# Optimization experiments

Measured on AMD Instinct MI355X. Metric: run time of the kernel, lower is better.

## Reference

```python
import jax, jax.numpy as jnp
import numpy as np

N, E, F_IN, C, H, B = 50000, 1600000, 64, 64, 2, 64
EPS_BN = 1e-5
NEG_SLOPE = 0.2


def setup_inputs() -> dict:
    key = jax.random.key(0)
    ks = jax.random.split(key, 20)
    s_in = 1.0 / np.sqrt(F_IN)
    s_c = 1.0 / np.sqrt(C)
    inp = {
        "x": jax.random.normal(ks[0], (N, F_IN), jnp.float32),
        "edge_index": jax.random.randint(ks[1], (2, E), 0, N, jnp.int32),
        "batch_index": jnp.sort(jax.random.randint(ks[2], (N,), 0, B, jnp.int32)),
        # GAT layer 1
        "W1": jax.random.normal(ks[3], (F_IN, H * C), jnp.float32) * s_in,
        "att_src1": jax.random.normal(ks[4], (H, C), jnp.float32) * s_c,
        "att_dst1": jax.random.normal(ks[5], (H, C), jnp.float32) * s_c,
        "bias1": jnp.zeros((C,), jnp.float32),
        # skip linear
        "skipW": jax.random.normal(ks[6], (F_IN, C), jnp.float32) * s_in,
        "skipb": jnp.zeros((C,), jnp.float32),
        # BN1
        "gamma1": jnp.ones((C,), jnp.float32),
        "beta1": jnp.zeros((C,), jnp.float32),
        # GAT layer 2
        "W2": jax.random.normal(ks[7], (C, H * C), jnp.float32) * s_c,
        "att_src2": jax.random.normal(ks[8], (H, C), jnp.float32) * s_c,
        "att_dst2": jax.random.normal(ks[9], (H, C), jnp.float32) * s_c,
        "bias2": jnp.zeros((C,), jnp.float32),
        # BN2
        "gamma2": jnp.ones((C,), jnp.float32),
        "beta2": jnp.zeros((C,), jnp.float32),
    }
    return inp


def _gat_conv(x, W, att_src, att_dst, bias, src, dst):
    # PyG GATConv with concat=False (mean over heads), self-loops already in src/dst
    n = x.shape[0]
    h = (x @ W).reshape(n, H, C)                           # [N,H,C]
    a_s = jnp.einsum("nhc,hc->nh", h, att_src)              # [N,H]
    a_d = jnp.einsum("nhc,hc->nh", h, att_dst)
    logits = jax.nn.leaky_relu(a_s[src] + a_d[dst], NEG_SLOPE)  # [E,H]
    m = jax.ops.segment_max(logits, dst, num_segments=n)    # scatter-softmax
    e = jnp.exp(logits - m[dst])
    denom = jax.ops.segment_sum(e, dst, num_segments=n)
    alpha = e / denom[dst]                                  # [E,H]
    msg = h[src] * alpha[:, :, None]                        # [E,H,C]
    out = jax.ops.segment_sum(msg, dst, num_segments=n)     # [N,H,C]
    return out.mean(axis=1) + bias                          # concat=False -> head mean


def _bn(x, gamma, beta):
    # BatchNorm1d, training mode (batch statistics, biased var)
    mu = x.mean(axis=0)
    var = x.var(axis=0)
    return (x - mu) * jax.lax.rsqrt(var + EPS_BN) * gamma + beta


def reference(x, edge_index, batch_index, W1, att_src1, att_dst1, bias1,
              skipW, skipb, gamma1, beta1, W2, att_src2, att_dst2, bias2,
              gamma2, beta2):
    n = x.shape[0]
    loops = jnp.arange(n, dtype=edge_index.dtype)
    src = jnp.concatenate([edge_index[0], loops])  # add_self_loops=True (PyG default)
    dst = jnp.concatenate([edge_index[1], loops])

    h = _gat_conv(x, W1, att_src1, att_dst1, bias1, src, dst)
    h = _bn(h, gamma1, beta1)
    h = jax.nn.gelu(h + x @ skipW + skipb)          # dropout = identity (eval)

    h2 = _gat_conv(h, W2, att_src2, att_dst2, bias2, src, dst)
    h2 = _bn(h2, gamma2, beta2)
    h2 = jax.nn.gelu(h2 + h)

    # global_mean_pool
    sums = jax.ops.segment_sum(h2, batch_index, num_segments=B)
    cnts = jax.ops.segment_sum(jnp.ones((n,), h2.dtype), batch_index, num_segments=B)
    return sums / jnp.maximum(cnts, 1.0)[:, None]   # [B, C]
```

## Files before the change

### kernel.cpp

```cpp
#include <hip/hip_runtime.h>
#include <math.h>


__device__ __forceinline__ float lrelu(float x){ return x > 0.f ? x : 0.2f*x; }
__device__ __forceinline__ float gelu_tanh(float x){
  const float k0 = 0.7978845608028654f;
  const float k1 = 0.044715f;
  float t = tanhf(k0 * fmaf(k1*x*x, x, x));
  return 0.5f*x*(1.f + t);
}
__device__ __forceinline__ unsigned short f2bf(float f){
  unsigned int u = __float_as_uint(f);
  u = (u + 0x7fffu + ((u >> 16) & 1u)) >> 16;
  return (unsigned short)u;
}
__device__ __forceinline__ float bf2f(unsigned short u){
  return __uint_as_float((unsigned int)u << 16);
}
__device__ __forceinline__ float bflo(unsigned int u){ return __uint_as_float(u << 16); }
__device__ __forceinline__ float bfhi(unsigned int u){ return __uint_as_float(u & 0xffff0000u); }
__device__ __forceinline__ unsigned int packbf(float a, float b){
  return ((unsigned int)f2bf(b) << 16) | (unsigned int)f2bf(a);
}
__device__ __forceinline__ unsigned char f2fp8(float v){
  return (unsigned char)(__builtin_amdgcn_cvt_pk_fp8_f32(v, v, 0, false) & 0xff);
}
typedef __attribute__((ext_vector_type(2))) float f32x2;

typedef __attribute__((ext_vector_type(8))) short bf16x8;
typedef __attribute__((ext_vector_type(4))) float f32x4;

__global__ void k_zero(float* __restrict__ p, int n){
  int i = blockIdx.x*blockDim.x + threadIdx.x;
  if (i < n) p[i] = 0.f;
}

__global__ void p_hist(const int* __restrict__ dst, int* __restrict__ bhist,
                       int E, int NB){
  __shared__ int lh[512];
  for (int i = threadIdx.x; i < NB; i += blockDim.x) lh[i] = 0;
  __syncthreads();
  int stride = gridDim.x * blockDim.x;
  for (int i = blockIdx.x*blockDim.x + threadIdx.x; i < E; i += stride)
    atomicAdd(&lh[dst[i] >> 7], 1);
  __syncthreads();
  for (int i = threadIdx.x; i < NB; i += blockDim.x)
    if (lh[i]) atomicAdd(&bhist[i], lh[i]);
}

__global__ void p_scan(const int* __restrict__ bhist, int* __restrict__ boff,
                       int* __restrict__ bcur, int* __restrict__ ptr,
                       int NB, int N, int E){
  __shared__ int ls[512];
  int t = threadIdx.x;
  int v = (t < NB) ? bhist[t] : 0;
  ls[t] = v; __syncthreads();
  for (int o = 1; o < 512; o <<= 1){
    int y = (t >= o) ? ls[t-o] : 0;
    __syncthreads();
    ls[t] += y;
    __syncthreads();
  }
  int ex = ls[t] - v;
  if (t < NB){ boff[t] = ex; bcur[t] = ex; }
  if (t == 0){ boff[NB] = E; ptr[N] = E; }
}

#define BIN_CHUNK 2048
__global__ void p_bin(const int* __restrict__ src, const int* __restrict__ dst,
                      int* __restrict__ bcur, unsigned int* __restrict__ recs,
                      int E, int NB){
  __shared__ int lh[512];
  __shared__ int lbase[512];
  int c0 = blockIdx.x * BIN_CHUNK;
  int cnt = min(BIN_CHUNK, E - c0);
  if (cnt <= 0) return;
  int t = threadIdx.x;
  for (int i = t; i < NB; i += blockDim.x) lh[i] = 0;
  __syncthreads();
  for (int i = t; i < cnt; i += blockDim.x)
    atomicAdd(&lh[dst[c0+i] >> 7], 1);
  __syncthreads();
  for (int i = t; i < NB; i += blockDim.x){
    int c = lh[i];
    lbase[i] = (c > 0) ? atomicAdd(&bcur[i], c) : 0;
    lh[i] = 0;
  }
  __syncthreads();
  for (int i = t; i < cnt; i += blockDim.x){
    int d = dst[c0+i];
    int b = d >> 7;
    int p = atomicAdd(&lh[b], 1);
    recs[lbase[b] + p] = ((unsigned int)src[c0+i] << 7) | (unsigned int)(d & 127);
  }
}

__global__ void p_csr(const unsigned int* __restrict__ recs, const int* __restrict__ boff,
                      int* __restrict__ ptr, int* __restrict__ srcs, int N){
  int b = blockIdx.x;
  int r0 = boff[b], r1 = boff[b+1];
  __shared__ int lh[128];
  int t = threadIdx.x;
  if (t < 128) lh[t] = 0;
  __syncthreads();
  for (int i = r0 + t; i < r1; i += 256)
    atomicAdd(&lh[recs[i] & 127u], 1);
  __syncthreads();
  int mycnt = (t < 128) ? lh[t] : 0;
  for (int o = 1; o < 128; o <<= 1){
    int y = (t < 128 && t >= o) ? lh[t-o] : 0;
    __syncthreads();
    if (t < 128) lh[t] += y;
    __syncthreads();
  }
  if (t < 128){
    int excl = lh[t] - mycnt;
    int node = b*128 + t;
    if (node < N) ptr[node] = r0 + excl;
    lh[t] = excl;
  }
  __syncthreads();
  for (int i = r0 + t; i < r1; i += 256){
    unsigned int rec = recs[i];
    int j = rec & 127u;
    int p = atomicAdd(&lh[j], 1);
    srcs[r0 + p] = (int)(rec >> 7);
  }
}

__global__ void k_gemm3(const float* __restrict__ X, const float* __restrict__ Wm,
                        const float* __restrict__ Wsk, const float* __restrict__ att_s,
                        const float* __restrict__ att_d, unsigned char* __restrict__ Hout,
                        unsigned short* __restrict__ skv, float* __restrict__ a_s,
                        float* __restrict__ a_d, int N){
  constexpr int NT = 12;
  __shared__ unsigned short Bl[NT*2*64*8];
  int t = threadIdx.x;
  const int TOT = 64 * 192;
  for (int e = t; e < TOT; e += 256){
    int k = e / 192, c = e % 192;
    float w = (c < 128) ? Wm[(size_t)k*128 + c] : Wsk[(size_t)k*64 + (c-128)];
    int ct = c >> 4;
    int h = k >> 5, kk = k & 31;
    int e2 = ((kk >> 4) << 2) | (kk & 3);
    int l  = (c & 15) | (((kk >> 2) & 3) << 4);
    Bl[(((ct*2 + h)*64) + l)*8 + e2] = f2bf(w);
  }
  __syncthreads();

  int lane = t & 63, wav = t >> 6;
  int m = lane & 15, g = lane >> 4;
  float asv[8], adv[8];
  #pragma unroll
  for (int ct = 0; ct < 8; ct++){ asv[ct] = att_s[ct*16 + m]; adv[ct] = att_d[ct*16 + m]; }

  #pragma unroll
  for (int it = 0; it < 2; it++){
    int rbase = blockIdx.x*128 + it*64 + wav*16;
    if (rbase >= N) break;
    int r = min(rbase + m, N-1);
    const float* xr = X + (size_t)r*64;
    float4 u0 = *(const float4*)(xr + g*4);
    float4 u1 = *(const float4*)(xr + 16 + g*4);
    float4 u2 = *(const float4*)(xr + 32 + g*4);
    float4 u3 = *(const float4*)(xr + 48 + g*4);
    bf16x8 a0, a1;
    a0[0]=(short)f2bf(u0.x); a0[1]=(short)f2bf(u0.y); a0[2]=(short)f2bf(u0.z); a0[3]=(short)f2bf(u0.w);
    a0[4]=(short)f2bf(u1.x); a0[5]=(short)f2bf(u1.y); a0[6]=(short)f2bf(u1.z); a0[7]=(short)f2bf(u1.w);
    a1[0]=(short)f2bf(u2.x); a1[1]=(short)f2bf(u2.y); a1[2]=(short)f2bf(u2.z); a1[3]=(short)f2bf(u2.w);
    a1[4]=(short)f2bf(u3.x); a1[5]=(short)f2bf(u3.y); a1[6]=(short)f2bf(u3.z); a1[7]=(short)f2bf(u3.w);

    f32x4 acc[NT];
    #pragma unroll
    for (int ct = 0; ct < NT; ct++) acc[ct] = (f32x4){0.f,0.f,0.f,0.f};
    #pragma unroll
    for (int ct = 0; ct < NT; ct++){
      bf16x8 b0 = *(const bf16x8*)&Bl[((ct*2+0)*64 + lane)*8];
      bf16x8 b1 = *(const bf16x8*)&Bl[((ct*2+1)*64 + lane)*8];
      acc[ct] = __builtin_amdgcn_mfma_f32_16x16x32_bf16(a0, b0, acc[ct], 0, 0, 0);
      acc[ct] = __builtin_amdgcn_mfma_f32_16x16x32_bf16(a1, b1, acc[ct], 0, 0, 0);
    }

    float ds0[4]={0,0,0,0}, dd0[4]={0,0,0,0}, ds1[4]={0,0,0,0}, dd1[4]={0,0,0,0};
    #pragma unroll
    for (int ct = 0; ct < 8; ct++){
      #pragma unroll
      for (int q = 0; q < 4; q++){
        float v = acc[ct][q];
        if (ct < 4){ ds0[q] = fmaf(v, asv[ct], ds0[q]); dd0[q] = fmaf(v, adv[ct], dd0[q]); }
        else       { ds1[q] = fmaf(v, asv[ct], ds1[q]); dd1[q] = fmaf(v, adv[ct], dd1[q]); }
      }
    }
    #pragma unroll
    for (int off = 1; off < 16; off <<= 1){
      #pragma unroll
      for (int q = 0; q < 4; q++){
        ds0[q] += __shfl_xor(ds0[q], off); dd0[q] += __shfl_xor(dd0[q], off);
        ds1[q] += __shfl_xor(ds1[q], off); dd1[q] += __shfl_xor(dd1[q], off);
      }
    }
    if (m == 0){
      #pragma unroll
      for (int q = 0; q < 4; q++){
        int rr = rbase + g*4 + q;
        if (rr < N){
          float2 s2; s2.x = ds0[q]; s2.y = ds1[q]; ((float2*)a_s)[rr] = s2;
          float2 d2; d2.x = dd0[q]; d2.y = dd1[q]; ((float2*)a_d)[rr] = d2;
        }
      }
    }
    #pragma unroll
    for (int ct = 0; ct < 8; ct++){
      #pragma unroll
      for (int q = 0; q < 4; q++){
        int rr = rbase + g*4 + q;
        if (rr < N) Hout[(size_t)rr*128 + ct*16 + m] = f2fp8(acc[ct][q]);
      }
    }
    #pragma unroll
    for (int ct = 8; ct < NT; ct++){
      #pragma unroll
      for (int q = 0; q < 4; q++){
        int rr = rbase + g*4 + q;
        if (rr < N) skv[(size_t)rr*64 + (ct-8)*16 + m] = f2bf(acc[ct][q]);
      }
    }
  }
}

__global__ void k_gemm2f(const unsigned short* __restrict__ gout, const unsigned short* __restrict__ skv,
                         const float* __restrict__ part, const float* __restrict__ gamma,
                         const float* __restrict__ beta, const float* __restrict__ skb,
                         const float* __restrict__ W2, const float* __restrict__ att_s,
                         const float* __restrict__ att_d,
                         unsigned char* __restrict__ Hout, unsigned short* __restrict__ hmid,
                         float* __restrict__ a_s, float* __restrict__ a_d,
                         int N, float invN){
  constexpr int NT = 8;
  __shared__ unsigned short Bl[NT*2*64*8];
  __shared__ float scs[64], shs[64];
  int t = threadIdx.x;
  if (t < 64){
    float mu  = part[t] * invN;
    float var = fmaxf(part[64+t] * invN - mu*mu, 0.f);
    float sc  = gamma[t] * rsqrtf(var + 1e-5f);
    scs[t] = sc;
    shs[t] = beta[t] - mu*sc + skb[t];
  }
  const int TOT = 64 * 128;
  for (int e = t; e < TOT; e += 256){
    int k = e >> 7, c = e & 127;
    float w = W2[(size_t)k*128 + c];
    int ct = c >> 4;
    int h = k >> 5, kk = k & 31;
    int e2 = ((kk >> 4) << 2) | (kk & 3);
    int l  = (c & 15) | (((kk >> 2) & 3) << 4);
    Bl[(((ct*2 + h)*64) + l)*8 + e2] = f2bf(w);
  }
  __syncthreads();

  int lane = t & 63, wav = t >> 6;
  int m = lane & 15, g = lane >> 4;
  float asv[8], adv[8];
  #pragma unroll
  for (int ct = 0; ct < 8; ct++){ asv[ct] = att_s[ct*16 + m]; adv[ct] = att_d[ct*16 + m]; }

  #pragma unroll
  for (int it = 0; it < 2; it++){
    int rbase = blockIdx.x*128 + it*64 + wav*16;
    if (rbase >= N) break;
    int rm = rbase + m;
    int r = min(rm, N-1);
    const unsigned short* gr = gout + (size_t)r*64;
    const unsigned short* sr = skv + (size_t)r*64;
    float hv[16];
    #pragma unroll
    for (int j = 0; j < 4; j++){
      int c0 = j*16 + g*4;
      uint2 gp = *(const uint2*)(gr + c0);
      uint2 sp = *(const uint2*)(sr + c0);
      float4 sc4 = *(const float4*)(&scs[c0]);
      float4 sh4 = *(const float4*)(&shs[c0]);
      float v0 = gelu_tanh(fmaf(bflo(gp.x), sc4.x, sh4.x) + bflo(sp.x));
      float v1 = gelu_tanh(fmaf(bfhi(gp.x), sc4.y, sh4.y) + bfhi(sp.x));
      float v2 = gelu_tanh(fmaf(bflo(gp.y), sc4.z, sh4.z) + bflo(sp.y));
      float v3 = gelu_tanh(fmaf(bfhi(gp.y), sc4.w, sh4.w) + bfhi(sp.y));
      hv[4*j+0] = v0; hv[4*j+1] = v1; hv[4*j+2] = v2; hv[4*j+3] = v3;
      if (rm < N){
        uint2 hp; hp.x = packbf(v0, v1); hp.y = packbf(v2, v3);
        *(uint2*)(hmid + (size_t)rm*64 + c0) = hp;
      }
    }
    bf16x8 a0, a1;
    #pragma unroll
    for (int i2 = 0; i2 < 8; i2++) a0[i2] = (short)f2bf(hv[i2]);
    #pragma unroll
    for (int i2 = 0; i2 < 8; i2++) a1[i2] = (short)f2bf(hv[8+i2]);

    f32x4 acc[NT];
    #pragma unroll
    for (int ct = 0; ct < NT; ct++) acc[ct] = (f32x4){0.f,0.f,0.f,0.f};
    #pragma unroll
    for (int ct = 0; ct < NT; ct++){
      bf16x8 b0 = *(const bf16x8*)&Bl[((ct*2+0)*64 + lane)*8];
      bf16x8 b1 = *(const bf16x8*)&Bl[((ct*2+1)*64 + lane)*8];
      acc[ct] = __builtin_amdgcn_mfma_f32_16x16x32_bf16(a0, b0, acc[ct], 0, 0, 0);
      acc[ct] = __builtin_amdgcn_mfma_f32_16x16x32_bf16(a1, b1, acc[ct], 0, 0, 0);
    }

    float ds0[4]={0,0,0,0}, dd0[4]={0,0,0,0}, ds1[4]={0,0,0,0}, dd1[4]={0,0,0,0};
    #pragma unroll
    for (int ct = 0; ct < 8; ct++){
      #pragma unroll
      for (int q = 0; q < 4; q++){
        float v = acc[ct][q];
        if (ct < 4){ ds0[q] = fmaf(v, asv[ct], ds0[q]); dd0[q] = fmaf(v, adv[ct], dd0[q]); }
        else       { ds1[q] = fmaf(v, asv[ct], ds1[q]); dd1[q] = fmaf(v, adv[ct], dd1[q]); }
      }
    }
    #pragma unroll
    for (int off = 1; off < 16; off <<= 1){
      #pragma unroll
      for (int q = 0; q < 4; q++){
        ds0[q] += __shfl_xor(ds0[q], off); dd0[q] += __shfl_xor(dd0[q], off);
        ds1[q] += __shfl_xor(ds1[q], off); dd1[q] += __shfl_xor(dd1[q], off);
      }
    }
    if (m == 0){
      #pragma unroll
      for (int q = 0; q < 4; q++){
        int rr = rbase + g*4 + q;
        if (rr < N){
          float2 s2; s2.x = ds0[q]; s2.y = ds1[q]; ((float2*)a_s)[rr] = s2;
          float2 d2; d2.x = dd0[q]; d2.y = dd1[q]; ((float2*)a_d)[rr] = d2;
        }
      }
    }
    #pragma unroll
    for (int ct = 0; ct < 8; ct++){
      #pragma unroll
      for (int q = 0; q < 4; q++){
        int rr = rbase + g*4 + q;
        if (rr < N) Hout[(size_t)rr*128 + ct*16 + m] = f2fp8(acc[ct][q]);
      }
    }
  }
}

__global__ void k_agg(const unsigned char* __restrict__ Hp, const float* __restrict__ a_s,
                      const float* __restrict__ a_d, const int* __restrict__ ptr,
                      const int* __restrict__ srcs, const float* __restrict__ bias,
                      unsigned int* __restrict__ out, int N){
  __shared__ unsigned int sbuf[4][64];
  __shared__ float wbuf[4][2][64];
  int tid = threadIdx.x;
  int wv = tid >> 6;
  int wid = (blockIdx.x*blockDim.x + tid) >> 6;
  int lane = tid & 63;
  if (wid >= N) return;
  int n = wid;
  const char* HB = (const char*)Hp;
  const float2* AS2 = (const float2*)a_s;
  float2 adv = ((const float2*)a_d)[n];
  float2 asv = AS2[n];
  int e0 = ptr[n], e1 = ptr[n+1];
  float w0 = __expf(lrelu(asv.x + adv.x));
  float w1 = __expf(lrelu(asv.y + adv.y));
  unsigned lane2 = (unsigned)lane << 1;
  unsigned int hw = *(const unsigned short*)(HB + (((unsigned)n << 7) | lane2));
  f32x2 hv = __builtin_amdgcn_cvt_pk_f32_fp8((int)hw, false);
  float wsel = (lane < 32) ? w0 : w1;
  float acc0 = hv.x * wsel;
  float acc1 = hv.y * wsel;
  float d0 = 0.f, d1 = 0.f;
  int hsel = lane >> 5;
  for (int base = e0; base < e1; base += 64){
    int i = base + lane;
    float e_0 = 0.f, e_1 = 0.f; unsigned sv = 0;
    if (i < e1){
      sv = (unsigned)srcs[i];
      float2 av = AS2[sv];
      e_0 = __expf(lrelu(av.x + adv.x));
      e_1 = __expf(lrelu(av.y + adv.y));
    }
    d0 += e_0; d1 += e_1;
    sbuf[wv][lane] = sv << 7;
    wbuf[wv][0][lane] = e_0;
    wbuf[wv][1][lane] = e_1;
    int cnt = min(64, e1 - base);
    #pragma unroll 8
    for (int j = 0; j < cnt; j++){
      unsigned off = sbuf[wv][j];
      float wss = wbuf[wv][hsel][j];
      unsigned int hj = *(const unsigned short*)(HB + (off | lane2));
      f32x2 h2 = __builtin_amdgcn_cvt_pk_f32_fp8((int)hj, false);
      acc0 = fmaf(h2.x, wss, acc0);
      acc1 = fmaf(h2.y, wss, acc1);
    }
  }
  #pragma unroll
  for (int o=32;o>0;o>>=1){ d0 += __shfl_xor(d0,o); d1 += __shfl_xor(d1,o); }
  d0 += w0; d1 += w1;
  float dsel = (lane < 32) ? d0 : d1;
  acc0 /= dsel; acc1 /= dsel;
  float o0 = 0.5f*(acc0 + __shfl_xor(acc0, 32));
  float o1 = 0.5f*(acc1 + __shfl_xor(acc1, 32));
  if (lane < 32){
    float vx = o0 + bias[2*lane];
    float vy = o1 + bias[2*lane+1];
    out[(size_t)n*32 + lane] = packbf(vx, vy);
  }
}

__global__ void k_bnstats(const unsigned short* __restrict__ X, float* __restrict__ part, int N){
  int t = threadIdx.x; int c = t & 63; int sub = t >> 6;
  float s = 0.f, s2 = 0.f;
  for (int r = blockIdx.x*4 + sub; r < N; r += gridDim.x*4){
    float v = bf2f(X[(size_t)r*64 + c]);
    s += v; s2 = fmaf(v, v, s2);
  }
  __shared__ float ls[256], lq[256];
  ls[t] = s; lq[t] = s2; __syncthreads();
  if (t < 64){
    s  = ls[t] + ls[t+64] + ls[t+128] + ls[t+192];
    s2 = lq[t] + lq[t+64] + lq[t+128] + lq[t+192];
    atomicAdd(&part[t], s);
    atomicAdd(&part[64+t], s2);
  }
}

__global__ void k_fusepool(const unsigned short* __restrict__ g2, const float* __restrict__ part,
                           const float* __restrict__ gamma, const float* __restrict__ beta,
                           const unsigned short* __restrict__ hmid, const int* __restrict__ batch,
                           float* __restrict__ pool, float* __restrict__ cnt, int N, float invN){
  int t = threadIdx.x; int c = t & 63; int sub = t >> 6;
  int r0 = blockIdx.x*64;
  float mu  = part[c] * invN;
  float var = fmaxf(part[64+c] * invN - mu*mu, 0.f);
  float scale = gamma[c] * rsqrtf(var + 1e-5f);
  float shift = beta[c] - mu*scale;
  float acc = 0.f, ca = 0.f; int curb = -1;
  for (int r = r0 + sub; r < N && r < r0 + 64; r += 4){
    int b = batch[r];
    if (b != curb){
      if (curb >= 0){
        atomicAdd(&pool[curb*64 + c], acc);
        if (c == 0) atomicAdd(&cnt[curb], ca);
      }
      acc = 0.f; ca = 0.f; curb = b;
    }
    float gv = bf2f(g2[(size_t)r*64 + c]);
    float hv = bf2f(hmid[(size_t)r*64 + c]);
    float v = gelu_tanh(fmaf(gv, scale, shift) + hv);
    acc += v; ca += 1.f;
  }
  if (curb >= 0){
    atomicAdd(&pool[curb*64 + c], acc);
    if (c == 0) atomicAdd(&cnt[curb], ca);
  }
}

__global__ void k_out(const float* __restrict__ pool, const float* __restrict__ cnt,
                      float* __restrict__ out, int M){
  int i = blockIdx.x*blockDim.x + threadIdx.x;
  if (i < M) out[i] = pool[i] / fmaxf(cnt[i>>6], 1.f);
}

extern "C" void kernel_launch(void* const* d_in, const int* in_sizes, int n_in,
                              void* d_out, int out_size, void* d_ws, size_t ws_size,
                              hipStream_t stream) {
  const float* x     = (const float*)d_in[0];
  const int*   ei    = (const int*)  d_in[1];
  const int*   batch = (const int*)  d_in[2];
  const float* W1    = (const float*)d_in[3];
  const float* as1   = (const float*)d_in[4];
  const float* ad1   = (const float*)d_in[5];
  const float* b1    = (const float*)d_in[6];
  const float* skW   = (const float*)d_in[7];
  const float* skb   = (const float*)d_in[8];
  const float* gm1   = (const float*)d_in[9];
  const float* bt1   = (const float*)d_in[10];
  const float* W2    = (const float*)d_in[11];
  const float* as2   = (const float*)d_in[12];
  const float* ad2   = (const float*)d_in[13];
  const float* b2    = (const float*)d_in[14];
  const float* gm2   = (const float*)d_in[15];
  const float* bt2   = (const float*)d_in[16];

  int N = in_sizes[2];
  int E = in_sizes[1] / 2;
  const int* esrc = ei;
  const int* edst = ei + E;
  int NB = (N + 127) >> 7;
  float invN = 1.0f / (float)N;

  char* wp = (char*)d_ws;
  size_t off = 0;
  auto alloc = [&](size_t bytes)->void*{
    off = (off + 255) & ~(size_t)255;
    void* p = wp + off;
    off += bytes;
    return p;
  };
  int*   ptr   = (int*)  alloc((size_t)(N+1)*4);
  int*   srcs  = (int*)  alloc((size_t)E*4);
  unsigned int* recs = (unsigned int*)alloc((size_t)E*4);
  int*   boff  = (int*)  alloc(520*4);
  int*   bcur  = (int*)  alloc(512*4);
  unsigned char* hpack = (unsigned char*)alloc((size_t)N*128);
  float* a_s  = (float*)alloc((size_t)N*2*4);
  float* a_d  = (float*)alloc((size_t)N*2*4);
  unsigned short* gout = (unsigned short*)alloc((size_t)N*64*2);
  unsigned short* skv  = (unsigned short*)alloc((size_t)N*64*2);
  unsigned short* hmid = (unsigned short*)alloc((size_t)N*64*2);
  const int ZN = 128+128+4096+64+512;
  float* zz   = (float*)alloc((size_t)ZN*4);
  float* part1 = zz;
  float* part2 = zz + 128;
  float* pool  = zz + 256;
  float* cnt   = zz + 256 + 4096;
  int*   bhist = (int*)(zz + 256 + 4096 + 64);

  int gg = (N + 127) / 128;

  k_zero<<<(ZN + 255)/256, 256, 0, stream>>>(zz, ZN);

  p_hist<<<512, 256, 0, stream>>>(edst, bhist, E, NB);
  p_scan<<<1, 512, 0, stream>>>(bhist, boff, bcur, ptr, NB, N, E);
  p_bin<<<(E + BIN_CHUNK - 1)/BIN_CHUNK, 256, 0, stream>>>(esrc, edst, bcur, recs, E, NB);
  p_csr<<<NB, 256, 0, stream>>>(recs, boff, ptr, srcs, N);

  k_gemm3<<<gg, 256, 0, stream>>>(x, W1, skW, as1, ad1, hpack, skv, a_s, a_d, N);
  k_agg<<<(N+3)/4, 256, 0, stream>>>(hpack, a_s, a_d, ptr, srcs, b1, (unsigned int*)gout, N);
  k_bnstats<<<256, 256, 0, stream>>>(gout, part1, N);

  k_gemm2f<<<gg, 256, 0, stream>>>(gout, skv, part1, gm1, bt1, skb, W2, as2, ad2,
                                   hpack, hmid, a_s, a_d, N, invN);
  k_agg<<<(N+3)/4, 256, 0, stream>>>(hpack, a_s, a_d, ptr, srcs, b2, (unsigned int*)gout, N);
  k_bnstats<<<256, 256, 0, stream>>>(gout, part2, N);

  k_fusepool<<<(N+63)/64, 256, 0, stream>>>(gout, part2, gm2, bt2, hmid, batch, pool, cnt, N, invN);
  k_out<<<(out_size + 255)/256, 256, 0, stream>>>(pool, cnt, (float*)d_out, out_size);
}
```

Baseline: 258.0 us.

## Process two edges per iteration in aggregation with wider fp8 loads; retune CSR binning

The aggregation kernel now splits each wavefront into two halves that handle alternating edges. Each lane loads four fp8 features with a 32-bit load instead of two with a 16-bit load, which halves the serial inner-loop trip count per node. Partial sums are combined across the halves with shuffles before the softmax normalization and head mean. Separately, CSR binning now uses a fixed 256 blocks of 512 threads with larger chunks, and the histogram grid is halved, to cut the number of global atomics on the bucket cursors.

Result: slower. 264.3 us (+2.5%).

```diff
diff --git a/kernel.cpp b/kernel.cpp
--- a/kernel.cpp
+++ b/kernel.cpp
@@ -66,14 +66,15 @@
   if (t == 0){ boff[NB] = E; ptr[N] = E; }
 }
 
-#define BIN_CHUNK 2048
+#define PBIN_BLOCKS 256
 __global__ void p_bin(const int* __restrict__ src, const int* __restrict__ dst,
                       int* __restrict__ bcur, unsigned int* __restrict__ recs,
                       int E, int NB){
   __shared__ int lh[512];
   __shared__ int lbase[512];
-  int c0 = blockIdx.x * BIN_CHUNK;
-  int cnt = min(BIN_CHUNK, E - c0);
+  int per = (E + PBIN_BLOCKS - 1) / PBIN_BLOCKS;
+  int c0 = blockIdx.x * per;
+  int cnt = min(per, E - c0);
   if (cnt <= 0) return;
   int t = threadIdx.x;
   for (int i = t; i < NB; i += blockDim.x) lh[i] = 0;
@@ -366,14 +367,17 @@
   int e0 = ptr[n], e1 = ptr[n+1];
   float w0 = __expf(lrelu(asv.x + adv.x));
   float w1 = __expf(lrelu(asv.y + adv.y));
-  unsigned lane2 = (unsigned)lane << 1;
-  unsigned int hw = *(const unsigned short*)(HB + (((unsigned)n << 7) | lane2));
-  f32x2 hv = __builtin_amdgcn_cvt_pk_f32_fp8((int)hw, false);
-  float wsel = (lane < 32) ? w0 : w1;
-  float acc0 = hv.x * wsel;
-  float acc1 = hv.y * wsel;
+  int half = lane >> 5;
+  int q    = lane & 31;
+  int hsel = q >> 4;
+  unsigned qb = (unsigned)q << 2;
+  unsigned int hw = *(const unsigned int*)(HB + (((unsigned)n << 7) | qb));
+  f32x2 s01 = __builtin_amdgcn_cvt_pk_f32_fp8((int)hw, false);
+  f32x2 s23 = __builtin_amdgcn_cvt_pk_f32_fp8((int)hw, true);
+  float wself = (half == 0) ? ((hsel == 0) ? w0 : w1) : 0.f;
+  float acc0 = s01.x * wself, acc1 = s01.y * wself;
+  float acc2 = s23.x * wself, acc3 = s23.y * wself;
   float d0 = 0.f, d1 = 0.f;
-  int hsel = lane >> 5;
   for (int base = e0; base < e1; base += 64){
     int i = base + lane;
     float e_0 = 0.f, e_1 = 0.f; unsigned sv = 0;
@@ -389,26 +393,38 @@
     wbuf[wv][1][lane] = e_1;
     int cnt = min(64, e1 - base);
     #pragma unroll 8
-    for (int j = 0; j < cnt; j++){
-      unsigned off = sbuf[wv][j];
-      float wss = wbuf[wv][hsel][j];
-      unsigned int hj = *(const unsigned short*)(HB + (off | lane2));
-      f32x2 h2 = __builtin_amdgcn_cvt_pk_f32_fp8((int)hj, false);
-      acc0 = fmaf(h2.x, wss, acc0);
-      acc1 = fmaf(h2.y, wss, acc1);
+    for (int j = 0; j < cnt; j += 2){
+      int jj = j + half;
+      unsigned off = sbuf[wv][jj];
+      float wss = wbuf[wv][hsel][jj];
+      unsigned int hj = *(const unsigned int*)(HB + (off | qb));
+      f32x2 h01 = __builtin_amdgcn_cvt_pk_f32_fp8((int)hj, false);
+      f32x2 h23 = __builtin_amdgcn_cvt_pk_f32_fp8((int)hj, true);
+      acc0 = fmaf(h01.x, wss, acc0);
+      acc1 = fmaf(h01.y, wss, acc1);
+      acc2 = fmaf(h23.x, wss, acc2);
+      acc3 = fmaf(h23.y, wss, acc3);
     }
   }
   #pragma unroll
   for (int o=32;o>0;o>>=1){ d0 += __shfl_xor(d0,o); d1 += __shfl_xor(d1,o); }
   d0 += w0; d1 += w1;
-  float dsel = (lane < 32) ? d0 : d1;
-  acc0 /= dsel; acc1 /= dsel;
-  float o0 = 0.5f*(acc0 + __shfl_xor(acc0, 32));
-  float o1 = 0.5f*(acc1 + __shfl_xor(acc1, 32));
-  if (lane < 32){
-    float vx = o0 + bias[2*lane];
-    float vy = o1 + bias[2*lane+1];
-    out[(size_t)n*32 + lane] = packbf(vx, vy);
+  acc0 += __shfl_xor(acc0, 32);
+  acc1 += __shfl_xor(acc1, 32);
+  acc2 += __shfl_xor(acc2, 32);
+  acc3 += __shfl_xor(acc3, 32);
+  float dsel = (hsel == 0) ? d0 : d1;
+  acc0 /= dsel; acc1 /= dsel; acc2 /= dsel; acc3 /= dsel;
+  float m0 = 0.5f*(acc0 + __shfl_xor(acc0, 16));
+  float m1 = 0.5f*(acc1 + __shfl_xor(acc1, 16));
+  float m2 = 0.5f*(acc2 + __shfl_xor(acc2, 16));
+  float m3 = 0.5f*(acc3 + __shfl_xor(acc3, 16));
+  if (half == 0 && q < 16){
+    float4 b4 = *(const float4*)(bias + 4*q);
+    uint2 res;
+    res.x = packbf(m0 + b4.x, m1 + b4.y);
+    res.y = packbf(m2 + b4.z, m3 + b4.w);
+    *(uint2*)(out + (size_t)n*32 + 2*q) = res;
   }
 }
 
@@ -525,9 +541,9 @@
 
   k_zero<<<(ZN + 255)/256, 256, 0, stream>>>(zz, ZN);
 
-  p_hist<<<512, 256, 0, stream>>>(edst, bhist, E, NB);
+  p_hist<<<256, 256, 0, stream>>>(edst, bhist, E, NB);
   p_scan<<<1, 512, 0, stream>>>(bhist, boff, bcur, ptr, NB, N, E);
-  p_bin<<<(E + BIN_CHUNK - 1)/BIN_CHUNK, 256, 0, stream>>>(esrc, edst, bcur, recs, E, NB);
+  p_bin<<<PBIN_BLOCKS, 512, 0, stream>>>(esrc, edst, bcur, recs, E, NB);
   p_csr<<<NB, 256, 0, stream>>>(recs, boff, ptr, srcs, N);
 
   k_gemm3<<<gg, 256, 0, stream>>>(x, W1, skW, as1, ad1, hpack, skv, a_s, a_d, N);
```
